# Performance work log

Hardware: AMD Instinct MI355X
Metric: run time of the kernel (lower is better)

Reference implementation:

```python
import jax, jax.numpy as jnp
import numpy as np

N_NODES = 10000
N_EDGES = 640000
D = 128


def setup_inputs() -> dict:
    key = jax.random.key(0)
    ks = jax.random.split(key, 8)
    x = jax.random.normal(ks[0], (N_NODES, D), dtype=jnp.float32)
    edge_weight = jax.random.uniform(ks[1], (N_EDGES,), dtype=jnp.float32)
    W0 = jax.random.normal(ks[2], (D, D), dtype=jnp.float32) * (1.0 / np.sqrt(D))
    b0 = jnp.zeros((D,), dtype=jnp.float32)
    W1 = jax.random.normal(ks[3], (D, D), dtype=jnp.float32) * (1.0 / np.sqrt(D))
    b1 = jnp.zeros((D,), dtype=jnp.float32)
    src = jax.random.randint(ks[4], (N_EDGES,), 0, N_NODES)
    dst = jax.random.randint(ks[5], (N_EDGES,), 0, N_NODES)
    return {"x": x, "edge_weight": edge_weight, "W0": W0, "b0": b0,
            "W1": W1, "b1": b1, "src": src, "dst": dst}


def _graph_conv(h, src, dst, edge_weight, W, b):
    # DGL GraphConv with norm='both', bias, activation=relu.
    n = h.shape[0]
    ones = jnp.ones((src.shape[0],), dtype=h.dtype)
    out_deg = jax.ops.segment_sum(ones, src, num_segments=n)
    in_deg = jax.ops.segment_sum(ones, dst, num_segments=n)
    norm_src = jax.lax.rsqrt(jnp.maximum(out_deg, 1.0))  # [N]
    norm_dst = jax.lax.rsqrt(jnp.maximum(in_deg, 1.0))   # [N]
    h = h * norm_src[:, None]
    # gather -> weight edges -> scatter-add (sparse neighbor aggregation)
    msg = h[src] * edge_weight[:, None]                  # [E, D]
    agg = jax.ops.segment_sum(msg, dst, num_segments=n)  # [N, D]
    rst = agg @ W                                        # in_feats == out_feats: aggregate first
    rst = rst * norm_dst[:, None] + b
    return jax.nn.relu(rst)  # activation inside GraphConv


def reference(x, edge_weight, W0, b0, W1, b1, src, dst):
    # NET.forward (full-graph path): per layer GraphConv -> activation -> dropout.
    # Dropout is identity in eval mode; outer relu after GraphConv's internal relu is idempotent
    # but applied for faithfulness.
    h = jax.nn.relu(_graph_conv(x, src, dst, edge_weight, W0, b0))
    h = jax.nn.relu(_graph_conv(h, src, dst, edge_weight, W1, b1))
    return h  # predict is None (n_classes=None)
```

## Files before the change

### kernel.cpp

```cpp
#include <hip/hip_runtime.h>
#include <hip/hip_fp16.h>

#define D 128
#define NB 256
#define Q 8
#define BQ (NB / Q)
#define NBINS_MAX 10016
#define GM 32

__global__ __launch_bounds__(256) void hist_kernel(const int* __restrict__ src, const int* __restrict__ dst,
                                                   const float* __restrict__ x, __half* __restrict__ xh, int total4,
                                                   int* __restrict__ pd, unsigned short* __restrict__ ps,
                                                   int E, int n) {
    __shared__ __align__(16) int hd[NBINS_MAX];
    __shared__ __align__(16) int hs[NBINS_MAX];
    int b = blockIdx.x, t = threadIdx.x;
    for (int i = b * 256 + t; i < total4; i += NB * 256) {
        float4 v = *(const float4*)(x + (size_t)i * 4);
        __half2 a = __floats2half2_rn(v.x, v.y);
        __half2 c = __floats2half2_rn(v.z, v.w);
        *(__half2*)(xh + (size_t)i * 4) = a;
        *(__half2*)(xh + (size_t)i * 4 + 2) = c;
    }
    int chunk = (E + NB - 1) / NB;
    int e0 = b * chunk, e1 = min(e0 + chunk, E);
    int nq = (n + 3) >> 2;
    for (int i = t; i < nq; i += 256) {
        *(int4*)(&hd[i * 4]) = make_int4(0, 0, 0, 0);
        *(int4*)(&hs[i * 4]) = make_int4(0, 0, 0, 0);
    }
    __syncthreads();
    for (int e = e0 + t; e < e1; e += 256) {
        atomicAdd(&hd[dst[e]], 1);
        atomicAdd(&hs[src[e]], 1);
    }
    __syncthreads();
    int nf = n >> 2;
    for (int i = t; i < nf; i += 256) {
        int4 h = *(const int4*)(&hd[i * 4]);
        *(int4*)(pd + (size_t)b * n + i * 4) = h;
        int4 s = *(const int4*)(&hs[i * 4]);
        uint2 u;
        u.x = (unsigned)(s.x & 0xFFFF) | ((unsigned)(s.y & 0xFFFF) << 16);
        u.y = (unsigned)(s.z & 0xFFFF) | ((unsigned)(s.w & 0xFFFF) << 16);
        *(uint2*)(ps + (size_t)b * n + i * 4) = u;
    }
    for (int i = nf * 4 + t; i < n; i += 256) {
        pd[(size_t)b * n + i] = hd[i];
        ps[(size_t)b * n + i] = (unsigned short)hs[i];
    }
}

__global__ __launch_bounds__(256) void colscan_kernel(int* __restrict__ pd, const unsigned short* __restrict__ ps,
                                                      int* __restrict__ qtot_d, int* __restrict__ qtot_s, int n) {
    int bin4 = (blockIdx.x * 256 + threadIdx.x) * 4;
    int q = blockIdx.y;
    if (bin4 >= n) return;
    int b0 = q * BQ;
    if (bin4 + 3 < n) {
        int4 run = make_int4(0, 0, 0, 0);
        int4 ssum = make_int4(0, 0, 0, 0);
#pragma unroll 8
        for (int j = 0; j < BQ; ++j) {
            size_t idx = (size_t)(b0 + j) * n + bin4;
            int4 v = *(const int4*)(pd + idx);
            *(int4*)(pd + idx) = run;
            run.x += v.x; run.y += v.y; run.z += v.z; run.w += v.w;
            uint2 u = *(const uint2*)(ps + idx);
            ssum.x += (int)(u.x & 0xFFFF); ssum.y += (int)(u.x >> 16);
            ssum.z += (int)(u.y & 0xFFFF); ssum.w += (int)(u.y >> 16);
        }
        *(int4*)(qtot_d + (size_t)q * n + bin4) = run;
        *(int4*)(qtot_s + (size_t)q * n + bin4) = ssum;
    } else {
        for (int bin = bin4; bin < n; ++bin) {
            int run = 0, ssum = 0;
            for (int j = 0; j < BQ; ++j) {
                size_t idx = (size_t)(b0 + j) * n + bin;
                int v = pd[idx];
                pd[idx] = run;
                run += v;
                ssum += (int)ps[idx];
            }
            qtot_d[(size_t)q * n + bin] = run;
            qtot_s[(size_t)q * n + bin] = ssum;
        }
    }
}

__global__ __launch_bounds__(1024) void finscan_kernel(int* __restrict__ qtot_d, const int* __restrict__ qtot_s,
                                                       int* __restrict__ row_start,
                                                       float* __restrict__ norm_src, float* __restrict__ norm_dst,
                                                       int n) {
    __shared__ int deg[NBINS_MAX];
    __shared__ int part[1024];
    int t = threadIdx.x;
    for (int b4 = t * 4; b4 < n; b4 += 4096) {
        if (b4 + 3 < n) {
            int4 qv[Q];
#pragma unroll
            for (int q = 0; q < Q; ++q) qv[q] = *(const int4*)(qtot_d + (size_t)q * n + b4);
            int4 run = make_int4(0, 0, 0, 0);
#pragma unroll
            for (int q = 0; q < Q; ++q) {
                *(int4*)(qtot_d + (size_t)q * n + b4) = run;
                run.x += qv[q].x; run.y += qv[q].y; run.z += qv[q].z; run.w += qv[q].w;
            }
            *(int4*)(&deg[b4]) = run;
            norm_dst[b4 + 0] = rsqrtf(fmaxf((float)run.x, 1.0f));
            norm_dst[b4 + 1] = rsqrtf(fmaxf((float)run.y, 1.0f));
            norm_dst[b4 + 2] = rsqrtf(fmaxf((float)run.z, 1.0f));
            norm_dst[b4 + 3] = rsqrtf(fmaxf((float)run.w, 1.0f));
            int4 st = make_int4(0, 0, 0, 0);
#pragma unroll
            for (int q = 0; q < Q; ++q) {
                int4 v = *(const int4*)(qtot_s + (size_t)q * n + b4);
                st.x += v.x; st.y += v.y; st.z += v.z; st.w += v.w;
            }
            norm_src[b4 + 0] = rsqrtf(fmaxf((float)st.x, 1.0f));
            norm_src[b4 + 1] = rsqrtf(fmaxf((float)st.y, 1.0f));
            norm_src[b4 + 2] = rsqrtf(fmaxf((float)st.z, 1.0f));
            norm_src[b4 + 3] = rsqrtf(fmaxf((float)st.w, 1.0f));
        } else {
            for (int bin = b4; bin < n; ++bin) {
                int run = 0;
                for (int q = 0; q < Q; ++q) {
                    size_t i = (size_t)q * n + bin;
                    int v = qtot_d[i];
                    qtot_d[i] = run;
                    run += v;
                }
                deg[bin] = run;
                norm_dst[bin] = rsqrtf(fmaxf((float)run, 1.0f));
                int tot = 0;
                for (int q = 0; q < Q; ++q) tot += qtot_s[(size_t)q * n + bin];
                norm_src[bin] = rsqrtf(fmaxf((float)tot, 1.0f));
            }
        }
    }
    __syncthreads();
    int ipt = (n + 1023) / 1024;
    int lo = min(t * ipt, n), hi = min(lo + ipt, n);
    int s = 0;
    for (int i = lo; i < hi; ++i) s += deg[i];
    part[t] = s;
    __syncthreads();
    for (int off = 1; off < 1024; off <<= 1) {
        int v = 0;
        if (t >= off) v = part[t - off];
        __syncthreads();
        if (t >= off) part[t] += v;
        __syncthreads();
    }
    int run = part[t] - s;
    for (int i = lo; i < hi; ++i) {
        int v = deg[i];
        row_start[i] = run;
        run += v;
    }
    if (t == 1023) row_start[n] = part[1023];
}

__global__ __launch_bounds__(256) void fill_kernel(const int* __restrict__ src, const int* __restrict__ dst,
                                                   const float* __restrict__ ew, const float* __restrict__ ns,
                                                   const int* __restrict__ row_start, const int* __restrict__ qbase,
                                                   const int* __restrict__ pd,
                                                   int2* __restrict__ sorted, int E, int n) {
    __shared__ __align__(16) int cursor[NBINS_MAX];
    int b = blockIdx.x, t = threadIdx.x;
    int q = b / BQ;
    int chunk = (E + NB - 1) / NB;
    int e0 = b * chunk, e1 = min(e0 + chunk, E);
    int nf = n >> 2;
    for (int i = t; i < nf; i += 256) {
        int4 r = *(const int4*)(row_start + i * 4);
        int4 a = *(const int4*)(qbase + (size_t)q * n + i * 4);
        int4 c = *(const int4*)(pd + (size_t)b * n + i * 4);
        *(int4*)(&cursor[i * 4]) = make_int4(r.x + a.x + c.x, r.y + a.y + c.y,
                                             r.z + a.z + c.z, r.w + a.w + c.w);
    }
    for (int i = nf * 4 + t; i < n; i += 256)
        cursor[i] = row_start[i] + qbase[(size_t)q * n + i] + pd[(size_t)b * n + i];
    __syncthreads();
    for (int e = e0 + t; e < e1; e += 256) {
        int d = dst[e];
        int slot = atomicAdd(&cursor[d], 1);
        int s = src[e];
        int2 rec;
        rec.x = s;
        rec.y = __float_as_int(ew[e] * ns[s]);
        sorted[slot] = rec;
    }
}

__global__ __launch_bounds__(256) void agg_kernel(const __half* __restrict__ h, const int* __restrict__ row_start,
                                                  const int2* __restrict__ sorted, float* __restrict__ out, int n) {
    int wave = threadIdx.x >> 6;
    int lane = threadIdx.x & 63;
    int node = blockIdx.x * 4 + wave;
    if (node >= n) return;
    const __half2* hc = (const __half2*)h + lane;
    int beg = __builtin_amdgcn_readfirstlane(row_start[node]);
    int end = __builtin_amdgcn_readfirstlane(row_start[node + 1]);
    float accx = 0.f, accy = 0.f;
    int s = beg;
    if (s < end && (s & 1)) {
        int2 rr = sorted[s];
        float w = __int_as_float(rr.y);
        float2 f = __half22float2(hc[(size_t)rr.x << 6]);
        accx = fmaf(w, f.x, accx); accy = fmaf(w, f.y, accy);
        ++s;
    }
    int4 p0, p1, p2, p3, p4, p5, p6, p7;
    if (s + 16 <= end) {
        p0 = *(const int4*)(sorted + s);
        p1 = *(const int4*)(sorted + s + 2);
        p2 = *(const int4*)(sorted + s + 4);
        p3 = *(const int4*)(sorted + s + 6);
        p4 = *(const int4*)(sorted + s + 8);
        p5 = *(const int4*)(sorted + s + 10);
        p6 = *(const int4*)(sorted + s + 12);
        p7 = *(const int4*)(sorted + s + 14);
    }
    for (; s + 32 <= end; s += 16) {
        int4 q0 = *(const int4*)(sorted + s + 16);
        int4 q1 = *(const int4*)(sorted + s + 18);
        int4 q2 = *(const int4*)(sorted + s + 20);
        int4 q3 = *(const int4*)(sorted + s + 22);
        int4 q4 = *(const int4*)(sorted + s + 24);
        int4 q5 = *(const int4*)(sorted + s + 26);
        int4 q6 = *(const int4*)(sorted + s + 28);
        int4 q7 = *(const int4*)(sorted + s + 30);
        __half2 x0  = hc[(size_t)p0.x << 6];
        __half2 x1  = hc[(size_t)p0.z << 6];
        __half2 x2  = hc[(size_t)p1.x << 6];
        __half2 x3  = hc[(size_t)p1.z << 6];
        __half2 x4  = hc[(size_t)p2.x << 6];
        __half2 x5  = hc[(size_t)p2.z << 6];
        __half2 x6  = hc[(size_t)p3.x << 6];
        __half2 x7  = hc[(size_t)p3.z << 6];
        __half2 x8  = hc[(size_t)p4.x << 6];
        __half2 x9  = hc[(size_t)p4.z << 6];
        __half2 x10 = hc[(size_t)p5.x << 6];
        __half2 x11 = hc[(size_t)p5.z << 6];
        __half2 x12 = hc[(size_t)p6.x << 6];
        __half2 x13 = hc[(size_t)p6.z << 6];
        __half2 x14 = hc[(size_t)p7.x << 6];
        __half2 x15 = hc[(size_t)p7.z << 6];
        float2 f;
        f = __half22float2(x0);  accx = fmaf(__int_as_float(p0.y), f.x, accx); accy = fmaf(__int_as_float(p0.y), f.y, accy);
        f = __half22float2(x1);  accx = fmaf(__int_as_float(p0.w), f.x, accx); accy = fmaf(__int_as_float(p0.w), f.y, accy);
        f = __half22float2(x2);  accx = fmaf(__int_as_float(p1.y), f.x, accx); accy = fmaf(__int_as_float(p1.y), f.y, accy);
        f = __half22float2(x3);  accx = fmaf(__int_as_float(p1.w), f.x, accx); accy = fmaf(__int_as_float(p1.w), f.y, accy);
        f = __half22float2(x4);  accx = fmaf(__int_as_float(p2.y), f.x, accx); accy = fmaf(__int_as_float(p2.y), f.y, accy);
        f = __half22float2(x5);  accx = fmaf(__int_as_float(p2.w), f.x, accx); accy = fmaf(__int_as_float(p2.w), f.y, accy);
        f = __half22float2(x6);  accx = fmaf(__int_as_float(p3.y), f.x, accx); accy = fmaf(__int_as_float(p3.y), f.y, accy);
        f = __half22float2(x7);  accx = fmaf(__int_as_float(p3.w), f.x, accx); accy = fmaf(__int_as_float(p3.w), f.y, accy);
        f = __half22float2(x8);  accx = fmaf(__int_as_float(p4.y), f.x, accx); accy = fmaf(__int_as_float(p4.y), f.y, accy);
        f = __half22float2(x9);  accx = fmaf(__int_as_float(p4.w), f.x, accx); accy = fmaf(__int_as_float(p4.w), f.y, accy);
        f = __half22float2(x10); accx = fmaf(__int_as_float(p5.y), f.x, accx); accy = fmaf(__int_as_float(p5.y), f.y, accy);
        f = __half22float2(x11); accx = fmaf(__int_as_float(p5.w), f.x, accx); accy = fmaf(__int_as_float(p5.w), f.y, accy);
        f = __half22float2(x12); accx = fmaf(__int_as_float(p6.y), f.x, accx); accy = fmaf(__int_as_float(p6.y), f.y, accy);
        f = __half22float2(x13); accx = fmaf(__int_as_float(p6.w), f.x, accx); accy = fmaf(__int_as_float(p6.w), f.y, accy);
        f = __half22float2(x14); accx = fmaf(__int_as_float(p7.y), f.x, accx); accy = fmaf(__int_as_float(p7.y), f.y, accy);
        f = __half22float2(x15); accx = fmaf(__int_as_float(p7.w), f.x, accx); accy = fmaf(__int_as_float(p7.w), f.y, accy);
        p0 = q0; p1 = q1; p2 = q2; p3 = q3;
        p4 = q4; p5 = q5; p6 = q6; p7 = q7;
    }
    if (s + 16 <= end) {
        float2 f;
        f = __half22float2(hc[(size_t)p0.x << 6]); accx = fmaf(__int_as_float(p0.y), f.x, accx); accy = fmaf(__int_as_float(p0.y), f.y, accy);
        f = __half22float2(hc[(size_t)p0.z << 6]); accx = fmaf(__int_as_float(p0.w), f.x, accx); accy = fmaf(__int_as_float(p0.w), f.y, accy);
        f = __half22float2(hc[(size_t)p1.x << 6]); accx = fmaf(__int_as_float(p1.y), f.x, accx); accy = fmaf(__int_as_float(p1.y), f.y, accy);
        f = __half22float2(hc[(size_t)p1.z << 6]); accx = fmaf(__int_as_float(p1.w), f.x, accx); accy = fmaf(__int_as_float(p1.w), f.y, accy);
        f = __half22float2(hc[(size_t)p2.x << 6]); accx = fmaf(__int_as_float(p2.y), f.x, accx); accy = fmaf(__int_as_float(p2.y), f.y, accy);
        f = __half22float2(hc[(size_t)p2.z << 6]); accx = fmaf(__int_as_float(p2.w), f.x, accx); accy = fmaf(__int_as_float(p2.w), f.y, accy);
        f = __half22float2(hc[(size_t)p3.x << 6]); accx = fmaf(__int_as_float(p3.y), f.x, accx); accy = fmaf(__int_as_float(p3.y), f.y, accy);
        f = __half22float2(hc[(size_t)p3.z << 6]); accx = fmaf(__int_as_float(p3.w), f.x, accx); accy = fmaf(__int_as_float(p3.w), f.y, accy);
        f = __half22float2(hc[(size_t)p4.x << 6]); accx = fmaf(__int_as_float(p4.y), f.x, accx); accy = fmaf(__int_as_float(p4.y), f.y, accy);
        f = __half22float2(hc[(size_t)p4.z << 6]); accx = fmaf(__int_as_float(p4.w), f.x, accx); accy = fmaf(__int_as_float(p4.w), f.y, accy);
        f = __half22float2(hc[(size_t)p5.x << 6]); accx = fmaf(__int_as_float(p5.y), f.x, accx); accy = fmaf(__int_as_float(p5.y), f.y, accy);
        f = __half22float2(hc[(size_t)p5.z << 6]); accx = fmaf(__int_as_float(p5.w), f.x, accx); accy = fmaf(__int_as_float(p5.w), f.y, accy);
        f = __half22float2(hc[(size_t)p6.x << 6]); accx = fmaf(__int_as_float(p6.y), f.x, accx); accy = fmaf(__int_as_float(p6.y), f.y, accy);
        f = __half22float2(hc[(size_t)p6.z << 6]); accx = fmaf(__int_as_float(p6.w), f.x, accx); accy = fmaf(__int_as_float(p6.w), f.y, accy);
        f = __half22float2(hc[(size_t)p7.x << 6]); accx = fmaf(__int_as_float(p7.y), f.x, accx); accy = fmaf(__int_as_float(p7.y), f.y, accy);
        f = __half22float2(hc[(size_t)p7.z << 6]); accx = fmaf(__int_as_float(p7.w), f.x, accx); accy = fmaf(__int_as_float(p7.w), f.y, accy);
        s += 16;
    }
    if (s + 8 <= end) {
        int4 a0 = *(const int4*)(sorted + s);
        int4 a1 = *(const int4*)(sorted + s + 2);
        int4 a2 = *(const int4*)(sorted + s + 4);
        int4 a3 = *(const int4*)(sorted + s + 6);
        float2 f;
        f = __half22float2(hc[(size_t)a0.x << 6]); accx = fmaf(__int_as_float(a0.y), f.x, accx); accy = fmaf(__int_as_float(a0.y), f.y, accy);
        f = __half22float2(hc[(size_t)a0.z << 6]); accx = fmaf(__int_as_float(a0.w), f.x, accx); accy = fmaf(__int_as_float(a0.w), f.y, accy);
        f = __half22float2(hc[(size_t)a1.x << 6]); accx = fmaf(__int_as_float(a1.y), f.x, accx); accy = fmaf(__int_as_float(a1.y), f.y, accy);
        f = __half22float2(hc[(size_t)a1.z << 6]); accx = fmaf(__int_as_float(a1.w), f.x, accx); accy = fmaf(__int_as_float(a1.w), f.y, accy);
        f = __half22float2(hc[(size_t)a2.x << 6]); accx = fmaf(__int_as_float(a2.y), f.x, accx); accy = fmaf(__int_as_float(a2.y), f.y, accy);
        f = __half22float2(hc[(size_t)a2.z << 6]); accx = fmaf(__int_as_float(a2.w), f.x, accx); accy = fmaf(__int_as_float(a2.w), f.y, accy);
        f = __half22float2(hc[(size_t)a3.x << 6]); accx = fmaf(__int_as_float(a3.y), f.x, accx); accy = fmaf(__int_as_float(a3.y), f.y, accy);
        f = __half22float2(hc[(size_t)a3.z << 6]); accx = fmaf(__int_as_float(a3.w), f.x, accx); accy = fmaf(__int_as_float(a3.w), f.y, accy);
        s += 8;
    }
    for (; s + 2 <= end; s += 2) {
        int4 p = *(const int4*)(sorted + s);
        float2 f;
        f = __half22float2(hc[(size_t)p.x << 6]); accx = fmaf(__int_as_float(p.y), f.x, accx); accy = fmaf(__int_as_float(p.y), f.y, accy);
        f = __half22float2(hc[(size_t)p.z << 6]); accx = fmaf(__int_as_float(p.w), f.x, accx); accy = fmaf(__int_as_float(p.w), f.y, accy);
    }
    if (s < end) {
        int2 rr = sorted[s];
        float w = __int_as_float(rr.y);
        float2 f = __half22float2(hc[(size_t)rr.x << 6]);
        accx = fmaf(w, f.x, accx); accy = fmaf(w, f.y, accy);
    }
    float2 o; o.x = accx; o.y = accy;
    *(float2*)(out + ((size_t)node << 7) + lane * 2) = o;
}

template <int HALF_OUT>
__global__ __launch_bounds__(256) void gemm_kernel(const float* __restrict__ A, const float* __restrict__ W,
                                                   const float* __restrict__ bias, const float* __restrict__ norm_dst,
                                                   float* __restrict__ out, __half* __restrict__ out_h, int n) {
    __shared__ __align__(16) float sAT[D][GM + 2];
    int tid = threadIdx.x;
    int row0 = blockIdx.x * GM;
    for (int i = tid; i < GM * 32; i += 256) {
        int r = i >> 5;
        int kq = i & 31;
        int rr = row0 + r;
        float4 v = make_float4(0.f, 0.f, 0.f, 0.f);
        if (rr < n) v = *(const float4*)(A + (size_t)rr * D + kq * 4);
        sAT[kq * 4 + 0][r] = v.x;
        sAT[kq * 4 + 1][r] = v.y;
        sAT[kq * 4 + 2][r] = v.z;
        sAT[kq * 4 + 3][r] = v.w;
    }
    __syncthreads();
    int tx = tid & 15;
    int ty = tid >> 4;
    int c0 = tx * 8;
    int r0 = ty * 2;
    float acc0[8], acc1[8];
#pragma unroll
    for (int j = 0; j < 8; ++j) { acc0[j] = 0.f; acc1[j] = 0.f; }
    const float* Wk = W + c0;
#pragma unroll 4
    for (int k = 0; k < D; ++k) {
        float2 a = *(const float2*)&sAT[k][r0];
        float4 w0 = *(const float4*)(Wk);
        float4 w1 = *(const float4*)(Wk + 4);
        Wk += D;
        acc0[0] = fmaf(a.x, w0.x, acc0[0]);
        acc0[1] = fmaf(a.x, w0.y, acc0[1]);
        acc0[2] = fmaf(a.x, w0.z, acc0[2]);
        acc0[3] = fmaf(a.x, w0.w, acc0[3]);
        acc0[4] = fmaf(a.x, w1.x, acc0[4]);
        acc0[5] = fmaf(a.x, w1.y, acc0[5]);
        acc0[6] = fmaf(a.x, w1.z, acc0[6]);
        acc0[7] = fmaf(a.x, w1.w, acc0[7]);
        acc1[0] = fmaf(a.y, w0.x, acc1[0]);
        acc1[1] = fmaf(a.y, w0.y, acc1[1]);
        acc1[2] = fmaf(a.y, w0.z, acc1[2]);
        acc1[3] = fmaf(a.y, w0.w, acc1[3]);
        acc1[4] = fmaf(a.y, w1.x, acc1[4]);
        acc1[5] = fmaf(a.y, w1.y, acc1[5]);
        acc1[6] = fmaf(a.y, w1.z, acc1[6]);
        acc1[7] = fmaf(a.y, w1.w, acc1[7]);
    }
#pragma unroll 2
    for (int rr = 0; rr < 2; ++rr) {
        int r = row0 + r0 + rr;
        if (r >= n) continue;
        float* acc = rr ? acc1 : acc0;
        float nd = norm_dst[r];
        float o[8];
#pragma unroll
        for (int j = 0; j < 8; ++j) o[j] = fmaxf(fmaf(acc[j], nd, bias[c0 + j]), 0.f);
        if (HALF_OUT) {
            __half2 h0 = __floats2half2_rn(o[0], o[1]);
            __half2 h1 = __floats2half2_rn(o[2], o[3]);
            __half2 h2 = __floats2half2_rn(o[4], o[5]);
            __half2 h3 = __floats2half2_rn(o[6], o[7]);
            __half* p = out_h + (size_t)r * D + c0;
            *(__half2*)(p + 0) = h0;
            *(__half2*)(p + 2) = h1;
            *(__half2*)(p + 4) = h2;
            *(__half2*)(p + 6) = h3;
        } else {
            float4 o0 = make_float4(o[0], o[1], o[2], o[3]);
            float4 o1 = make_float4(o[4], o[5], o[6], o[7]);
            *(float4*)(out + (size_t)r * D + c0) = o0;
            *(float4*)(out + (size_t)r * D + c0 + 4) = o1;
        }
    }
}

extern "C" void kernel_launch(void* const* d_in, const int* in_sizes, int n_in,
                              void* d_out, int out_size, void* d_ws, size_t ws_size,
                              hipStream_t stream) {
    const float* x  = (const float*)d_in[0];
    const float* ew = (const float*)d_in[1];
    const float* W0 = (const float*)d_in[2];
    const float* b0 = (const float*)d_in[3];
    const float* W1 = (const float*)d_in[4];
    const float* b1 = (const float*)d_in[5];
    const int* src  = (const int*)d_in[6];
    const int* dst  = (const int*)d_in[7];
    float* out = (float*)d_out;

    int n = in_sizes[0] / D;
    int E = in_sizes[6];
    if (n <= 0 || E <= 0) return;

    char* ws = (char*)d_ws;
    size_t off = 0;
    auto alloc = [&](size_t bytes) -> void* {
        void* p = ws + off;
        off = (off + bytes + 255) & ~(size_t)255;
        return p;
    };
    int* row_start  = (int*)alloc(((size_t)n + 1) * 4);
    float* norm_src = (float*)alloc((size_t)n * 4);
    float* norm_dst = (float*)alloc((size_t)n * 4);
    int* qtot_d     = (int*)alloc((size_t)Q * n * 4);
    int* qtot_s     = (int*)alloc((size_t)Q * n * 4);
    int2* sorted    = (int2*)alloc((size_t)E * 8);
    int* pd         = (int*)alloc((size_t)NB * n * 4);
    unsigned short* ps = (unsigned short*)alloc((size_t)NB * n * 2);
    float* B1       = (float*)alloc((size_t)n * D * 4);
    __half* xh      = (__half*)alloc((size_t)n * D * 2);
    __half* B2h     = (__half*)alloc((size_t)n * D * 2);

    int nb4 = (n + 1023) / 1024;
    int ab = (n + 3) / 4;
    int gb = (n + GM - 1) / GM;

    hist_kernel<<<NB, 256, 0, stream>>>(src, dst, x, xh, n * D / 4, pd, ps, E, n);
    colscan_kernel<<<dim3(nb4, Q), 256, 0, stream>>>(pd, ps, qtot_d, qtot_s, n);
    finscan_kernel<<<1, 1024, 0, stream>>>(qtot_d, qtot_s, row_start, norm_src, norm_dst, n);
    fill_kernel<<<NB, 256, 0, stream>>>(src, dst, ew, norm_src, row_start, qtot_d, pd, sorted, E, n);

    agg_kernel<<<ab, 256, 0, stream>>>(xh, row_start, sorted, B1, n);
    gemm_kernel<1><<<gb, 256, 0, stream>>>(B1, W0, b0, norm_dst, nullptr, B2h, n);
    agg_kernel<<<ab, 256, 0, stream>>>(B2h, row_start, sorted, B1, n);
    gemm_kernel<0><<<gb, 256, 0, stream>>>(B1, W1, b1, norm_dst, out, nullptr, n);
}
```

Before: 186.5 us.

## Reorder second layer to transform-then-aggregate and fuse both GEMMs

Uses the linearity of aggregation: layer-2 computes h@W1 right after the layer-1 GEMM inside one fused kernel (kept in shared memory), then aggregates the transformed features with norm/bias/relu in the aggregation epilogue. This removes one GEMM launch and one full fp32 intermediate round-trip. The cost is that the rounding order changes, since the layer-2 product is stored in fp16 before aggregation, and the fused GEMM kernel holds two weight passes per block.

```diff
diff --git a/kernel.cpp b/kernel.cpp
--- a/kernel.cpp
+++ b/kernel.cpp
@@ -193,8 +193,11 @@
     }
 }
 
+template <int EPI>
 __global__ __launch_bounds__(256) void agg_kernel(const __half* __restrict__ h, const int* __restrict__ row_start,
-                                                  const int2* __restrict__ sorted, float* __restrict__ out, int n) {
+                                                  const int2* __restrict__ sorted, float* __restrict__ out,
+                                                  const float* __restrict__ norm_dst, const float* __restrict__ bias,
+                                                  int n) {
     int wave = threadIdx.x >> 6;
     int lane = threadIdx.x & 63;
     int node = blockIdx.x * 4 + wave;
@@ -315,14 +318,22 @@
         float2 f = __half22float2(hc[(size_t)rr.x << 6]);
         accx = fmaf(w, f.x, accx); accy = fmaf(w, f.y, accy);
     }
-    float2 o; o.x = accx; o.y = accy;
+    float2 o;
+    if (EPI) {
+        float nd = norm_dst[node];
+        o.x = fmaxf(fmaf(accx, nd, bias[lane * 2]), 0.f);
+        o.y = fmaxf(fmaf(accy, nd, bias[lane * 2 + 1]), 0.f);
+    } else {
+        o.x = accx; o.y = accy;
+    }
     *(float2*)(out + ((size_t)node << 7) + lane * 2) = o;
 }
 
-template <int HALF_OUT>
-__global__ __launch_bounds__(256) void gemm_kernel(const float* __restrict__ A, const float* __restrict__ W,
-                                                   const float* __restrict__ bias, const float* __restrict__ norm_dst,
-                                                   float* __restrict__ out, __half* __restrict__ out_h, int n) {
+__global__ __launch_bounds__(256) void gemmfused_kernel(const float* __restrict__ A,
+                                                        const float* __restrict__ W0, const float* __restrict__ b0,
+                                                        const float* __restrict__ W1,
+                                                        const float* __restrict__ norm_dst,
+                                                        __half* __restrict__ out_h, int n) {
     __shared__ __align__(16) float sAT[D][GM + 2];
     int tid = threadIdx.x;
     int row0 = blockIdx.x * GM;
@@ -345,55 +356,86 @@
     float acc0[8], acc1[8];
 #pragma unroll
     for (int j = 0; j < 8; ++j) { acc0[j] = 0.f; acc1[j] = 0.f; }
-    const float* Wk = W + c0;
+    {
+        const float* Wk = W0 + c0;
 #pragma unroll 4
-    for (int k = 0; k < D; ++k) {
-        float2 a = *(const float2*)&sAT[k][r0];
-        float4 w0 = *(const float4*)(Wk);
-        float4 w1 = *(const float4*)(Wk + 4);
-        Wk += D;
-        acc0[0] = fmaf(a.x, w0.x, acc0[0]);
-        acc0[1] = fmaf(a.x, w0.y, acc0[1]);
-        acc0[2] = fmaf(a.x, w0.z, acc0[2]);
-        acc0[3] = fmaf(a.x, w0.w, acc0[3]);
-        acc0[4] = fmaf(a.x, w1.x, acc0[4]);
-        acc0[5] = fmaf(a.x, w1.y, acc0[5]);
-        acc0[6] = fmaf(a.x, w1.z, acc0[6]);
-        acc0[7] = fmaf(a.x, w1.w, acc0[7]);
-        acc1[0] = fmaf(a.y, w0.x, acc1[0]);
-        acc1[1] = fmaf(a.y, w0.y, acc1[1]);
-        acc1[2] = fmaf(a.y, w0.z, acc1[2]);
-        acc1[3] = fmaf(a.y, w0.w, acc1[3]);
-        acc1[4] = fmaf(a.y, w1.x, acc1[4]);
-        acc1[5] = fmaf(a.y, w1.y, acc1[5]);
-        acc1[6] = fmaf(a.y, w1.z, acc1[6]);
-        acc1[7] = fmaf(a.y, w1.w, acc1[7]);
-    }
+        for (int k = 0; k < D; ++k) {
+            float2 a = *(const float2*)&sAT[k][r0];
+            float4 w0 = *(const float4*)(Wk);
+            float4 w1 = *(const float4*)(Wk + 4);
+            Wk += D;
+            acc0[0] = fmaf(a.x, w0.x, acc0[0]);
+            acc0[1] = fmaf(a.x, w0.y, acc0[1]);
+            acc0[2] = fmaf(a.x, w0.z, acc0[2]);
+            acc0[3] = fmaf(a.x, w0.w, acc0[3]);
+            acc0[4] = fmaf(a.x, w1.x, acc0[4]);
+            acc0[5] = fmaf(a.x, w1.y, acc0[5]);
+            acc0[6] = fmaf(a.x, w1.z, acc0[6]);
+            acc0[7] = fmaf(a.x, w1.w, acc0[7]);
+            acc1[0] = fmaf(a.y, w0.x, acc1[0]);
+            acc1[1] = fmaf(a.y, w0.y, acc1[1]);
+            acc1[2] = fmaf(a.y, w0.z, acc1[2]);
+            acc1[3] = fmaf(a.y, w0.w, acc1[3]);
+            acc1[4] = fmaf(a.y, w1.x, acc1[4]);
+            acc1[5] = fmaf(a.y, w1.y, acc1[5]);
+            acc1[6] = fmaf(a.y, w1.z, acc1[6]);
+            acc1[7] = fmaf(a.y, w1.w, acc1[7]);
+        }
+    }
+    __syncthreads();
 #pragma unroll 2
     for (int rr = 0; rr < 2; ++rr) {
         int r = row0 + r0 + rr;
         if (r >= n) continue;
         float* acc = rr ? acc1 : acc0;
         float nd = norm_dst[r];
-        float o[8];
-#pragma unroll
-        for (int j = 0; j < 8; ++j) o[j] = fmaxf(fmaf(acc[j], nd, bias[c0 + j]), 0.f);
-        if (HALF_OUT) {
-            __half2 h0 = __floats2half2_rn(o[0], o[1]);
-            __half2 h1 = __floats2half2_rn(o[2], o[3]);
-            __half2 h2 = __floats2half2_rn(o[4], o[5]);
-            __half2 h3 = __floats2half2_rn(o[6], o[7]);
-            __half* p = out_h + (size_t)r * D + c0;
-            *(__half2*)(p + 0) = h0;
-            *(__half2*)(p + 2) = h1;
-            *(__half2*)(p + 4) = h2;
-            *(__half2*)(p + 6) = h3;
-        } else {
-            float4 o0 = make_float4(o[0], o[1], o[2], o[3]);
-            float4 o1 = make_float4(o[4], o[5], o[6], o[7]);
-            *(float4*)(out + (size_t)r * D + c0) = o0;
-            *(float4*)(out + (size_t)r * D + c0 + 4) = o1;
+#pragma unroll
+        for (int j = 0; j < 8; ++j)
+            sAT[c0 + j][r0 + rr] = fmaxf(fmaf(acc[j], nd, b0[c0 + j]), 0.f);
+    }
+    __syncthreads();
+#pragma unroll
+    for (int j = 0; j < 8; ++j) { acc0[j] = 0.f; acc1[j] = 0.f; }
+    {
+        const float* Wk = W1 + c0;
+#pragma unroll 4
+        for (int k = 0; k < D; ++k) {
+            float2 a = *(const float2*)&sAT[k][r0];
+            float4 w0 = *(const float4*)(Wk);
+            float4 w1 = *(const float4*)(Wk + 4);
+            Wk += D;
+            acc0[0] = fmaf(a.x, w0.x, acc0[0]);
+            acc0[1] = fmaf(a.x, w0.y, acc0[1]);
+            acc0[2] = fmaf(a.x, w0.z, acc0[2]);
+            acc0[3] = fmaf(a.x, w0.w, acc0[3]);
+            acc0[4] = fmaf(a.x, w1.x, acc0[4]);
+            acc0[5] = fmaf(a.x, w1.y, acc0[5]);
+            acc0[6] = fmaf(a.x, w1.z, acc0[6]);
+            acc0[7] = fmaf(a.x, w1.w, acc0[7]);
+            acc1[0] = fmaf(a.y, w0.x, acc1[0]);
+            acc1[1] = fmaf(a.y, w0.y, acc1[1]);
+            acc1[2] = fmaf(a.y, w0.z, acc1[2]);
+            acc1[3] = fmaf(a.y, w0.w, acc1[3]);
+            acc1[4] = fmaf(a.y, w1.x, acc1[4]);
+            acc1[5] = fmaf(a.y, w1.y, acc1[5]);
+            acc1[6] = fmaf(a.y, w1.z, acc1[6]);
+            acc1[7] = fmaf(a.y, w1.w, acc1[7]);
         }
+    }
+#pragma unroll 2
+    for (int rr = 0; rr < 2; ++rr) {
+        int r = row0 + r0 + rr;
+        if (r >= n) continue;
+        float* acc = rr ? acc1 : acc0;
+        __half2 h0 = __floats2half2_rn(acc[0], acc[1]);
+        __half2 h1 = __floats2half2_rn(acc[2], acc[3]);
+        __half2 h2 = __floats2half2_rn(acc[4], acc[5]);
+        __half2 h3 = __floats2half2_rn(acc[6], acc[7]);
+        __half* p = out_h + (size_t)r * D + c0;
+        *(__half2*)(p + 0) = h0;
+        *(__half2*)(p + 2) = h1;
+        *(__half2*)(p + 4) = h2;
+        *(__half2*)(p + 6) = h3;
     }
 }
 
@@ -431,7 +473,7 @@
     unsigned short* ps = (unsigned short*)alloc((size_t)NB * n * 2);
     float* B1       = (float*)alloc((size_t)n * D * 4);
     __half* xh      = (__half*)alloc((size_t)n * D * 2);
-    __half* B2h     = (__half*)alloc((size_t)n * D * 2);
+    __half* th      = (__half*)alloc((size_t)n * D * 2);
 
     int nb4 = (n + 1023) / 1024;
     int ab = (n + 3) / 4;
@@ -442,8 +484,7 @@
     finscan_kernel<<<1, 1024, 0, stream>>>(qtot_d, qtot_s, row_start, norm_src, norm_dst, n);
     fill_kernel<<<NB, 256, 0, stream>>>(src, dst, ew, norm_src, row_start, qtot_d, pd, sorted, E, n);
 
-    agg_kernel<<<ab, 256, 0, stream>>>(xh, row_start, sorted, B1, n);
-    gemm_kernel<1><<<gb, 256, 0, stream>>>(B1, W0, b0, norm_dst, nullptr, B2h, n);
-    agg_kernel<<<ab, 256, 0, stream>>>(B2h, row_start, sorted, B1, n);
-    gemm_kernel<0><<<gb, 256, 0, stream>>>(B1, W1, b1, norm_dst, out, nullptr, n);
-}
+    agg_kernel<0><<<ab, 256, 0, stream>>>(xh, row_start, sorted, B1, nullptr, nullptr, n);
+    gemmfused_kernel<<<gb, 256, 0, stream>>>(B1, W0, b0, W1, norm_dst, th, n);
+    agg_kernel<1><<<ab, 256, 0, stream>>>(th, row_start, sorted, out, norm_dst, b1, n);
+}
```

Measured after the change: 182.4 us (median of 2 runs). -2.2%, faster.
